# Performance work log

Measured on AMD Instinct MI355X. Metric: run time of the kernel, lower is better.

## Reference

```python
import jax, jax.numpy as jnp
import numpy as np

B, T, E = 2, 2048, 1024
H = 16
D = E // H  # 64

def setup_inputs() -> dict:
    key = jax.random.key(0)
    kx, kq, kk, kv, ko = jax.random.split(key, 5)
    s = 1.0 / np.sqrt(E)
    return {
        "x":  jax.random.normal(kx, (B, T, E), dtype=jnp.float32),
        "Wq": jax.random.normal(kq, (E, E), dtype=jnp.float32) * s,
        "Wk": jax.random.normal(kk, (E, E), dtype=jnp.float32) * s,
        "Wv": jax.random.normal(kv, (E, E), dtype=jnp.float32) * s,
        "Wo": jax.random.normal(ko, (E, E), dtype=jnp.float32) * s,
    }

def reference(x, Wq, Wk, Wv, Wo):
    # Faithful to the torch module, including its quirks:
    #  - head split is a raw .view(B, H, T, D) reshape (NOT a transpose split)
    #  - masked_fill result is discarded in the original, so NO causal mask is applied
    #  - dropout = 0.0 -> identity
    b, t, e = x.shape
    q = jnp.reshape(x @ Wq, (b, H, t, D))
    k = jnp.reshape(x @ Wk, (b, H, t, D))
    v = jnp.reshape(x @ Wv, (b, H, t, D))
    # raw_score = q @ k^T ; softmax over keys of raw_score / sqrt(head_dim)
    scores = jnp.einsum("bhtd,bhsd->bhts", q, k) / jnp.sqrt(jnp.asarray(D, x.dtype))
    attn = jax.nn.softmax(scores, axis=-1)
    h = jnp.einsum("bhts,bhsd->bhtd", attn, v)           # (B,H,T,D)
    h = jnp.reshape(h, (b, t, e))                         # .view(B, T, -1)
    return h @ Wo
```

## Files before the change

### kernel.cpp

```cpp
#include <hip/hip_runtime.h>
#include <hip/hip_bf16.h>
#include <math.h>

#define BB 2
#define TT 2048
#define EE 1024
#define HH 16
#define DD 64
#define MM (BB*TT)

typedef __bf16 bf16;
typedef bf16 bf16x8 __attribute__((ext_vector_type(8)));
typedef bf16 bf16x4 __attribute__((ext_vector_type(4)));
typedef float f32x4 __attribute__((ext_vector_type(4)));

#define MFMA16(a,b,c) __builtin_amdgcn_mfma_f32_16x16x32_bf16((a),(b),(c),0,0,0)

__device__ __forceinline__ void gload_lds16(const void* g, void* l) {
  __builtin_amdgcn_global_load_lds(
      (const __attribute__((address_space(1))) unsigned int*)g,
      (__attribute__((address_space(3))) unsigned int*)l, 16, 0, 0);
}

__device__ __forceinline__ unsigned short bits(bf16 h) {
  return __builtin_bit_cast(unsigned short, h);
}

__global__ __launch_bounds__(256) void prep(const float* __restrict__ x,
                                            const float* __restrict__ w0,
                                            const float* __restrict__ w1,
                                            const float* __restrict__ w2,
                                            const float* __restrict__ w3,
                                            bf16* __restrict__ xb,
                                            bf16* t0, bf16* t1, bf16* t2, bf16* t3) {
  __shared__ bf16 tile[64][65];
  const int bid = blockIdx.x;
  if (bid < 4096) {
    const int i = bid * 256 + threadIdx.x;
    float4 f = ((const float4*)x)[i];
    bf16x4 h;
    h[0] = (bf16)f.x; h[1] = (bf16)f.y; h[2] = (bf16)f.z; h[3] = (bf16)f.w;
    ((bf16x4*)xb)[i] = h;
    return;
  }
  const int t = bid - 4096;
  const int z = t >> 8, rem = t & 255;
  const float* W = z == 0 ? w0 : z == 1 ? w1 : z == 2 ? w2 : w3;
  bf16* T = z == 0 ? t0 : z == 1 ? t1 : z == 2 ? t2 : t3;
  const int n0 = (rem & 15) * 64, k0 = (rem >> 4) * 64;
#pragma unroll
  for (int i = 0; i < 16; i++) {
    int idx = threadIdx.x + i * 256;
    int r = idx >> 6, c = idx & 63;
    tile[c][r] = (bf16)W[(size_t)(k0 + r) * EE + n0 + c];
  }
  __syncthreads();
#pragma unroll
  for (int i = 0; i < 16; i++) {
    int idx = threadIdx.x + i * 256;
    int r = idx >> 6, c = idx & 63;
    T[(size_t)(n0 + r) * EE + k0 + c] = tile[r][c];
  }
}

template <typename OutT>
__device__ __forceinline__ void gemm_core(const bf16* __restrict__ A, const bf16* __restrict__ Bt,
                                          OutT* __restrict__ C, bf16* As, bf16* Bs) {
  const int tid = threadIdx.x;
  const int w = tid >> 6, lane = tid & 63;
  const int lg = lane >> 4, lr = lane & 15;
  const int row0 = blockIdx.y * 128, col0 = blockIdx.x * 128;
  const int wrow = (w >> 1) * 64, wcol = (w & 1) * 64;
  f32x4 acc[4][4];
#pragma unroll
  for (int m = 0; m < 4; m++)
#pragma unroll
    for (int n = 0; n < 4; n++) acc[m][n] = f32x4{0.f, 0.f, 0.f, 0.f};

  for (int kt = 0; kt < EE; kt += 32) {
#pragma unroll
    for (int i = 0; i < 2; i++) {
      const int c = i * 4 + w;
      const int row = c * 16 + (lane >> 2);
      const int kof = (lane & 3) * 8;
      gload_lds16(A + (size_t)(row0 + row) * EE + kt + kof, &As[c * 512]);
      gload_lds16(Bt + (size_t)(col0 + row) * EE + kt + kof, &Bs[c * 512]);
    }
    __syncthreads();
    bf16x8 a[4], b[4];
#pragma unroll
    for (int m = 0; m < 4; m++)
      a[m] = *(const bf16x8*)&As[(wrow + m * 16 + lr) * 32 + lg * 8];
#pragma unroll
    for (int n = 0; n < 4; n++)
      b[n] = *(const bf16x8*)&Bs[(wcol + n * 16 + lr) * 32 + lg * 8];
#pragma unroll
    for (int m = 0; m < 4; m++)
#pragma unroll
      for (int n = 0; n < 4; n++) acc[m][n] = MFMA16(a[m], b[n], acc[m][n]);
    __syncthreads();
  }
#pragma unroll
  for (int m = 0; m < 4; m++)
#pragma unroll
    for (int n = 0; n < 4; n++)
#pragma unroll
      for (int r = 0; r < 4; r++) {
        const int rr = row0 + wrow + m * 16 + lg * 4 + r;
        const int cc = col0 + wcol + n * 16 + lr;
        C[(size_t)rr * EE + cc] = (OutT)acc[m][n][r];
      }
}

__global__ __launch_bounds__(256) void gemm_qkv(const bf16* __restrict__ A,
                                                const bf16* __restrict__ w0,
                                                const bf16* __restrict__ w1,
                                                const bf16* __restrict__ w2,
                                                bf16* o0, bf16* o1, bf16* o2) {
  __shared__ __align__(16) bf16 As[128 * 32];
  __shared__ __align__(16) bf16 Bs[128 * 32];
  const bf16* Bt = (blockIdx.z == 0) ? w0 : (blockIdx.z == 1) ? w1 : w2;
  bf16* C = (blockIdx.z == 0) ? o0 : (blockIdx.z == 1) ? o1 : o2;
  gemm_core<bf16>(A, Bt, C, As, Bs);
}

__global__ __launch_bounds__(256) void gemm_out(const bf16* __restrict__ A,
                                                const bf16* __restrict__ Bt,
                                                float* __restrict__ C) {
  __shared__ __align__(16) bf16 As[128 * 32];
  __shared__ __align__(16) bf16 Bs[128 * 32];
  gemm_core<float>(A, Bt, C, As, Bs);
}

__global__ __launch_bounds__(256, 2) void flash_attn(const bf16* __restrict__ Q,
                                                     const bf16* __restrict__ K,
                                                     const bf16* __restrict__ V,
                                                     bf16* __restrict__ Hout) {
  const int tid = threadIdx.x;
  const int w = tid >> 6, lane = tid & 63;
  const int hi = lane >> 4, lr = lane & 15;

  const int bid = blockIdx.x + 16 * blockIdx.y;
  const int sid = (bid & 7) * 64 + (bid >> 3);
  const int qb = sid & 15, bh = sid >> 4;

  const size_t base = (size_t)(bh >> 4) * TT * EE + (size_t)(bh & 15) * 128 * EE;
  const bf16* qh = Q + base;
  const bf16* kh = K + base;
  const bf16* vh = V + base;
  bf16* hh = Hout + base;
  const int r0w = qb * 128 + w * 32;

  __shared__ __align__(16) bf16 Ks[2][64 * 72];
  __shared__ __align__(16) bf16 Vt[2][64 * 72];

  const float qscale = 0.18033688011112042f;
  bf16x8 aq[2][2];
#pragma unroll
  for (int rg = 0; rg < 2; rg++)
#pragma unroll
    for (int kk = 0; kk < 2; kk++) {
      bf16x8 qv = *(const bf16x8*)(qh + (size_t)(r0w + rg * 16 + lr) * DD + kk * 32 + hi * 8);
#pragma unroll
      for (int j = 0; j < 8; j++) qv[j] = (bf16)(qscale * (float)qv[j]);
      aq[rg][kk] = qv;
    }

  float l_[2] = {0.f, 0.f};
  f32x4 o[2][4];
#pragma unroll
  for (int rg = 0; rg < 2; rg++)
#pragma unroll
    for (int d = 0; d < 4; d++) o[rg][d] = f32x4{0.f, 0.f, 0.f, 0.f};

  const int krow = tid >> 2, kg8 = (tid & 3) * 8;
  const int vsp = tid & 31, vdb = (tid >> 5) * 4;
  const int s0p = 2 * vsp;
  const int vcs = (s0p & 32) | (((s0p >> 2) & 3) << 3) | (((s0p >> 4) & 1) << 2) | (s0p & 3);

  bf16x8 kr0 = *(const bf16x8*)(kh + (size_t)krow * DD + kg8);
  bf16x8 kr1 = *(const bf16x8*)(kh + (size_t)krow * DD + kg8 + 32);
  bf16x4 va0 = *(const bf16x4*)(vh + (size_t)(2 * vsp) * DD + vdb);
  bf16x4 vb0 = *(const bf16x4*)(vh + (size_t)(2 * vsp + 1) * DD + vdb);
  bf16x4 va1 = *(const bf16x4*)(vh + (size_t)(2 * vsp) * DD + vdb + 32);
  bf16x4 vb1 = *(const bf16x4*)(vh + (size_t)(2 * vsp + 1) * DD + vdb + 32);
  *(bf16x8*)&Ks[0][krow * 72 + kg8] = kr0;
  *(bf16x8*)&Ks[0][krow * 72 + kg8 + 32] = kr1;
#pragma unroll
  for (int j = 0; j < 4; j++) {
    unsigned u0 = (unsigned)bits(va0[j]) | ((unsigned)bits(vb0[j]) << 16);
    unsigned u1 = (unsigned)bits(va1[j]) | ((unsigned)bits(vb1[j]) << 16);
    *(unsigned*)&Vt[0][(vdb + j) * 72 + vcs] = u0;
    *(unsigned*)&Vt[0][(vdb + 32 + j) * 72 + vcs] = u1;
  }
  kr0 = *(const bf16x8*)(kh + (size_t)(64 + krow) * DD + kg8);
  kr1 = *(const bf16x8*)(kh + (size_t)(64 + krow) * DD + kg8 + 32);
  va0 = *(const bf16x4*)(vh + (size_t)(64 + 2 * vsp) * DD + vdb);
  vb0 = *(const bf16x4*)(vh + (size_t)(64 + 2 * vsp + 1) * DD + vdb);
  va1 = *(const bf16x4*)(vh + (size_t)(64 + 2 * vsp) * DD + vdb + 32);
  vb1 = *(const bf16x4*)(vh + (size_t)(64 + 2 * vsp + 1) * DD + vdb + 32);
  __syncthreads();

  for (int t = 0; t < TT / 64; t++) {
    const bf16* Kc = Ks[t & 1];
    const bf16* Vc = Vt[t & 1];

    f32x4 sA[2][4];
#pragma unroll
    for (int rg = 0; rg < 2; rg++)
#pragma unroll
      for (int cf = 0; cf < 4; cf++) sA[rg][cf] = f32x4{0.f, 0.f, 0.f, 0.f};
#pragma unroll
    for (int cf = 0; cf < 4; cf++)
#pragma unroll
      for (int kk = 0; kk < 2; kk++) {
        bf16x8 bk = *(const bf16x8*)&Kc[(cf * 16 + lr) * 72 + kk * 32 + hi * 8];
#pragma unroll
        for (int rg = 0; rg < 2; rg++) sA[rg][cf] = MFMA16(bk, aq[rg][kk], sA[rg][cf]);
      }

    bf16x8 bp[2][2];
#pragma unroll
    for (int rg = 0; rg < 2; rg++) {
      f32x4 pr[4];
#pragma unroll
      for (int cf = 0; cf < 4; cf++)
#pragma unroll
        for (int r = 0; r < 4; r++) {
          float p = __builtin_amdgcn_exp2f(sA[rg][cf][r]);
          l_[rg] += p;
          pr[cf][r] = p;
        }
#pragma unroll
      for (int kk = 0; kk < 2; kk++)
#pragma unroll
        for (int j = 0; j < 8; j++)
          bp[rg][kk][j] = (bf16)pr[2 * kk + (j >> 2)][j & 3];
    }

#pragma unroll
    for (int kk = 0; kk < 2; kk++)
#pragma unroll
      for (int dblk = 0; dblk < 4; dblk++) {
        bf16x8 av = *(const bf16x8*)&Vc[(dblk * 16 + lr) * 72 + kk * 32 + hi * 8];
#pragma unroll
        for (int rg = 0; rg < 2; rg++)
          o[rg][dblk] = MFMA16(av, bp[rg][kk], o[rg][dblk]);
      }

    if (t < TT / 64 - 1) {
      bf16* Kn = Ks[(t + 1) & 1];
      bf16* Vn = Vt[(t + 1) & 1];
      *(bf16x8*)&Kn[krow * 72 + kg8] = kr0;
      *(bf16x8*)&Kn[krow * 72 + kg8 + 32] = kr1;
#pragma unroll
      for (int j = 0; j < 4; j++) {
        unsigned u0 = (unsigned)bits(va0[j]) | ((unsigned)bits(vb0[j]) << 16);
        unsigned u1 = (unsigned)bits(va1[j]) | ((unsigned)bits(vb1[j]) << 16);
        *(unsigned*)&Vn[(vdb + j) * 72 + vcs] = u0;
        *(unsigned*)&Vn[(vdb + 32 + j) * 72 + vcs] = u1;
      }
      if (t < TT / 64 - 2) {
        const int s2 = (t + 2) * 64;
        kr0 = *(const bf16x8*)(kh + (size_t)(s2 + krow) * DD + kg8);
        kr1 = *(const bf16x8*)(kh + (size_t)(s2 + krow) * DD + kg8 + 32);
        va0 = *(const bf16x4*)(vh + (size_t)(s2 + 2 * vsp) * DD + vdb);
        vb0 = *(const bf16x4*)(vh + (size_t)(s2 + 2 * vsp + 1) * DD + vdb);
        va1 = *(const bf16x4*)(vh + (size_t)(s2 + 2 * vsp) * DD + vdb + 32);
        vb1 = *(const bf16x4*)(vh + (size_t)(s2 + 2 * vsp + 1) * DD + vdb + 32);
      }
    }
    __syncthreads();
  }

#pragma unroll
  for (int rg = 0; rg < 2; rg++) {
    float lt = l_[rg];
    lt += __shfl_xor(lt, 16);
    lt += __shfl_xor(lt, 32);
#pragma unroll
    for (int dblk = 0; dblk < 4; dblk++) {
      bf16x4 st;
#pragma unroll
      for (int r = 0; r < 4; r++) st[r] = (bf16)(o[rg][dblk][r] / lt);
      *(bf16x4*)(hh + (size_t)(r0w + rg * 16 + lr) * DD + dblk * 16 + 4 * hi) = st;
    }
  }
}

extern "C" void kernel_launch(void* const* d_in, const int* in_sizes, int n_in,
                              void* d_out, int out_size, void* d_ws, size_t ws_size,
                              hipStream_t stream) {
  const float* x  = (const float*)d_in[0];
  const float* Wq = (const float*)d_in[1];
  const float* Wk = (const float*)d_in[2];
  const float* Wv = (const float*)d_in[3];
  const float* Wo = (const float*)d_in[4];
  float* out = (float*)d_out;

  bf16* xb  = (bf16*)d_ws;
  bf16* wqt = xb + (size_t)MM * EE;
  bf16* wkt = wqt + (size_t)EE * EE;
  bf16* wvt = wkt + (size_t)EE * EE;
  bf16* wot = wvt + (size_t)EE * EE;
  bf16* Qb  = wot + (size_t)EE * EE;
  bf16* Kb  = Qb + (size_t)MM * EE;
  bf16* Vb  = Kb + (size_t)MM * EE;
  bf16* Hb  = xb;

  prep<<<dim3(5120), 256, 0, stream>>>(x, Wq, Wk, Wv, Wo, xb, wqt, wkt, wvt, wot);
  gemm_qkv<<<dim3(8, 32, 3), 256, 0, stream>>>(xb, wqt, wkt, wvt, Qb, Kb, Vb);
  flash_attn<<<dim3(16, 32), 256, 0, stream>>>(Qb, Kb, Vb, Hb);
  gemm_out<<<dim3(8, 32), 256, 0, stream>>>(Hb, wot, out);
}
```

Baseline: 114.5 us.

## Split attention over two key halves and merge partial results

Flash attention now splits the key/value sequence into two halves across a third grid dimension, doubling the block count. Each block writes unnormalized fp32 partial outputs and row sums, and a new merge kernel sums the halves, normalizes and writes bf16. The aim is more resident waves per CU and better latency hiding, with launch bounds raised to allow four blocks per CU. In exchange it adds a sizable fp32 round trip through global memory and an extra launch. Merging by plain summation is only correct if both halves use the same fixed softmax offset rather than a per-half running max.

```diff
diff --git a/kernel.cpp b/kernel.cpp
--- a/kernel.cpp
+++ b/kernel.cpp
@@ -132,22 +132,27 @@
   gemm_core<float>(A, Bt, C, As, Bs);
 }
 
-__global__ __launch_bounds__(256, 2) void flash_attn(const bf16* __restrict__ Q,
-                                                     const bf16* __restrict__ K,
-                                                     const bf16* __restrict__ V,
-                                                     bf16* __restrict__ Hout) {
+template <bool PARTIAL>
+__global__ __launch_bounds__(256, PARTIAL ? 4 : 2)
+void flash_attn(const bf16* __restrict__ Q, const bf16* __restrict__ K,
+                const bf16* __restrict__ V, bf16* __restrict__ Hout,
+                float* __restrict__ Opart, float* __restrict__ Lpart) {
   const int tid = threadIdx.x;
   const int w = tid >> 6, lane = tid & 63;
   const int hi = lane >> 4, lr = lane & 15;
 
-  const int bid = blockIdx.x + 16 * blockIdx.y;
-  const int sid = (bid & 7) * 64 + (bid >> 3);
-  const int qb = sid & 15, bh = sid >> 4;
+  const int NB = PARTIAL ? 1024 : 512;
+  const int bid = blockIdx.x + 16 * blockIdx.y + (PARTIAL ? 512 * blockIdx.z : 0);
+  const int sid = (bid & 7) * (NB / 8) + (bid >> 3);
+  const int qb = sid & 15;
+  const int bh = (sid >> 4) & 31;
+  const int sh = PARTIAL ? (sid >> 9) : 0;
+  const int NT = PARTIAL ? (TT / 128) : (TT / 64);
 
   const size_t base = (size_t)(bh >> 4) * TT * EE + (size_t)(bh & 15) * 128 * EE;
   const bf16* qh = Q + base;
-  const bf16* kh = K + base;
-  const bf16* vh = V + base;
+  const bf16* kh = K + base + (size_t)sh * (TT / 2) * DD;
+  const bf16* vh = V + base + (size_t)sh * (TT / 2) * DD;
   bf16* hh = Hout + base;
   const int r0w = qb * 128 + w * 32;
 
@@ -201,7 +206,7 @@
   vb1 = *(const bf16x4*)(vh + (size_t)(64 + 2 * vsp + 1) * DD + vdb + 32);
   __syncthreads();
 
-  for (int t = 0; t < TT / 64; t++) {
+  for (int t = 0; t < NT; t++) {
     const bf16* Kc = Ks[t & 1];
     const bf16* Vc = Vt[t & 1];
 
@@ -248,7 +253,7 @@
           o[rg][dblk] = MFMA16(av, bp[rg][kk], o[rg][dblk]);
       }
 
-    if (t < TT / 64 - 1) {
+    if (t < NT - 1) {
       bf16* Kn = Ks[(t + 1) & 1];
       bf16* Vn = Vt[(t + 1) & 1];
       *(bf16x8*)&Kn[krow * 72 + kg8] = kr0;
@@ -260,7 +265,7 @@
         *(unsigned*)&Vn[(vdb + j) * 72 + vcs] = u0;
         *(unsigned*)&Vn[(vdb + 32 + j) * 72 + vcs] = u1;
       }
-      if (t < TT / 64 - 2) {
+      if (t < NT - 2) {
         const int s2 = (t + 2) * 64;
         kr0 = *(const bf16x8*)(kh + (size_t)(s2 + krow) * DD + kg8);
         kr1 = *(const bf16x8*)(kh + (size_t)(s2 + krow) * DD + kg8 + 32);
@@ -273,19 +278,59 @@
     __syncthreads();
   }
 
-#pragma unroll
-  for (int rg = 0; rg < 2; rg++) {
-    float lt = l_[rg];
-    lt += __shfl_xor(lt, 16);
-    lt += __shfl_xor(lt, 32);
-#pragma unroll
-    for (int dblk = 0; dblk < 4; dblk++) {
-      bf16x4 st;
-#pragma unroll
-      for (int r = 0; r < 4; r++) st[r] = (bf16)(o[rg][dblk][r] / lt);
-      *(bf16x4*)(hh + (size_t)(r0w + rg * 16 + lr) * DD + dblk * 16 + 4 * hi) = st;
-    }
-  }
+  if (PARTIAL) {
+    float* op = Opart + ((size_t)sh * 32 + bh) * TT * DD;
+    float* lp = Lpart + ((size_t)sh * 32 + bh) * TT;
+#pragma unroll
+    for (int rg = 0; rg < 2; rg++) {
+      const int q = r0w + rg * 16 + lr;
+      float lt = l_[rg];
+      lt += __shfl_xor(lt, 16);
+      lt += __shfl_xor(lt, 32);
+      if (hi == 0) lp[q] = lt;
+#pragma unroll
+      for (int dblk = 0; dblk < 4; dblk++)
+        *(f32x4*)&op[(size_t)q * DD + dblk * 16 + 4 * hi] = o[rg][dblk];
+    }
+  } else {
+#pragma unroll
+    for (int rg = 0; rg < 2; rg++) {
+      float lt = l_[rg];
+      lt += __shfl_xor(lt, 16);
+      lt += __shfl_xor(lt, 32);
+#pragma unroll
+      for (int dblk = 0; dblk < 4; dblk++) {
+        bf16x4 st;
+#pragma unroll
+        for (int r = 0; r < 4; r++) st[r] = (bf16)(o[rg][dblk][r] / lt);
+        *(bf16x4*)(hh + (size_t)(r0w + rg * 16 + lr) * DD + dblk * 16 + 4 * hi) = st;
+      }
+    }
+  }
+}
+
+__global__ __launch_bounds__(256) void merge_attn(const float* __restrict__ Opart,
+                                                  const float* __restrict__ Lpart,
+                                                  bf16* __restrict__ Hb) {
+  const int gid = blockIdx.x * 256 + threadIdx.x;
+  const int qg = gid >> 2;
+  const int d0 = (gid & 3) * 16;
+  const size_t off = (size_t)qg * DD + d0;
+  const size_t half = (size_t)32 * TT * DD;
+  const float inv = 1.0f / (Lpart[qg] + Lpart[32 * TT + qg]);
+  bf16x8 r0, r1;
+#pragma unroll
+  for (int v = 0; v < 4; v++) {
+    f32x4 a = *(const f32x4*)&Opart[off + v * 4];
+    f32x4 b = *(const f32x4*)&Opart[half + off + v * 4];
+#pragma unroll
+    for (int j = 0; j < 4; j++) {
+      bf16 x = (bf16)((a[j] + b[j]) * inv);
+      if (v < 2) r0[v * 4 + j] = x; else r1[(v - 2) * 4 + j] = x;
+    }
+  }
+  *(bf16x8*)&Hb[off] = r0;
+  *(bf16x8*)&Hb[off + 8] = r1;
 }
 
 extern "C" void kernel_launch(void* const* d_in, const int* in_sizes, int n_in,
@@ -308,8 +353,18 @@
   bf16* Vb  = Kb + (size_t)MM * EE;
   bf16* Hb  = xb;
 
+  const size_t base_bytes = ((size_t)MM * EE + 4 * (size_t)EE * EE + 3 * (size_t)MM * EE) * 2;
+  float* Opart = (float*)((char*)d_ws + base_bytes);
+  float* Lpart = Opart + (size_t)2 * 32 * TT * DD;
+  const size_t need = base_bytes + ((size_t)2 * 32 * TT * DD + (size_t)2 * 32 * TT) * 4;
+
   prep<<<dim3(5120), 256, 0, stream>>>(x, Wq, Wk, Wv, Wo, xb, wqt, wkt, wvt, wot);
   gemm_qkv<<<dim3(8, 32, 3), 256, 0, stream>>>(xb, wqt, wkt, wvt, Qb, Kb, Vb);
-  flash_attn<<<dim3(16, 32), 256, 0, stream>>>(Qb, Kb, Vb, Hb);
+  if (ws_size >= need) {
+    flash_attn<true><<<dim3(16, 32, 2), 256, 0, stream>>>(Qb, Kb, Vb, Hb, Opart, Lpart);
+    merge_attn<<<dim3(1024), 256, 0, stream>>>(Opart, Lpart, Hb);
+  } else {
+    flash_attn<false><<<dim3(16, 32), 256, 0, stream>>>(Qb, Kb, Vb, Hb, Opart, Lpart);
+  }
   gemm_out<<<dim3(8, 32), 256, 0, stream>>>(Hb, wot, out);
 }
```

Measured after the change: 126.1 us. +10.1%, slower.

## Split attention key blocks across wave pairs and retile output GEMM to 128x64

Applied to the files above, without the earlier changes.

In flash attention, each wave now covers 64 query rows and half of each 64-key block instead of 32 rows and the full block. This halves the per-wave LDS reads of K and V fragments. The two partial outputs and row sums are then combined through shared memory in an epilogue, which costs an extra barrier and LDS traffic at the end. Separately, the output projection GEMM uses a 128x64 tile with a grid twice as large, so more blocks are available to fill the CUs.

```diff
diff --git a/kernel.cpp b/kernel.cpp
--- a/kernel.cpp
+++ b/kernel.cpp
@@ -128,8 +128,53 @@
                                                 const bf16* __restrict__ Bt,
                                                 float* __restrict__ C) {
   __shared__ __align__(16) bf16 As[128 * 32];
-  __shared__ __align__(16) bf16 Bs[128 * 32];
-  gemm_core<float>(A, Bt, C, As, Bs);
+  __shared__ __align__(16) bf16 Bs[64 * 32];
+  const int tid = threadIdx.x;
+  const int w = tid >> 6, lane = tid & 63;
+  const int lg = lane >> 4, lr = lane & 15;
+  const int row0 = blockIdx.y * 128, col0 = blockIdx.x * 64;
+  const int wrow = (w >> 1) * 64, wcol = (w & 1) * 32;
+  f32x4 acc[4][2];
+#pragma unroll
+  for (int m = 0; m < 4; m++)
+#pragma unroll
+    for (int n = 0; n < 2; n++) acc[m][n] = f32x4{0.f, 0.f, 0.f, 0.f};
+
+  for (int kt = 0; kt < EE; kt += 32) {
+#pragma unroll
+    for (int i = 0; i < 3; i++) {
+      const int c = i * 4 + w;
+      const int r16 = lane >> 2, kof = (lane & 3) * 8;
+      if (c < 8)
+        gload_lds16(A + (size_t)(row0 + c * 16 + r16) * EE + kt + kof, &As[c * 512]);
+      else
+        gload_lds16(Bt + (size_t)(col0 + (c - 8) * 16 + r16) * EE + kt + kof,
+                    &Bs[(c - 8) * 512]);
+    }
+    __syncthreads();
+    bf16x8 a[4], b[2];
+#pragma unroll
+    for (int m = 0; m < 4; m++)
+      a[m] = *(const bf16x8*)&As[(wrow + m * 16 + lr) * 32 + lg * 8];
+#pragma unroll
+    for (int n = 0; n < 2; n++)
+      b[n] = *(const bf16x8*)&Bs[(wcol + n * 16 + lr) * 32 + lg * 8];
+#pragma unroll
+    for (int m = 0; m < 4; m++)
+#pragma unroll
+      for (int n = 0; n < 2; n++) acc[m][n] = MFMA16(a[m], b[n], acc[m][n]);
+    __syncthreads();
+  }
+#pragma unroll
+  for (int m = 0; m < 4; m++)
+#pragma unroll
+    for (int n = 0; n < 2; n++)
+#pragma unroll
+      for (int r = 0; r < 4; r++) {
+        const int rr = row0 + wrow + m * 16 + lg * 4 + r;
+        const int cc = col0 + wcol + n * 16 + lr;
+        C[(size_t)rr * EE + cc] = acc[m][n][r];
+      }
 }
 
 __global__ __launch_bounds__(256, 2) void flash_attn(const bf16* __restrict__ Q,
@@ -139,37 +184,39 @@
   const int tid = threadIdx.x;
   const int w = tid >> 6, lane = tid & 63;
   const int hi = lane >> 4, lr = lane & 15;
+  const int qh = w & 1, sh2 = w >> 1;
 
   const int bid = blockIdx.x + 16 * blockIdx.y;
   const int sid = (bid & 7) * 64 + (bid >> 3);
   const int qb = sid & 15, bh = sid >> 4;
 
   const size_t base = (size_t)(bh >> 4) * TT * EE + (size_t)(bh & 15) * 128 * EE;
-  const bf16* qh = Q + base;
+  const bf16* qh_p = Q + base;
   const bf16* kh = K + base;
   const bf16* vh = V + base;
   bf16* hh = Hout + base;
-  const int r0w = qb * 128 + w * 32;
-
-  __shared__ __align__(16) bf16 Ks[2][64 * 72];
-  __shared__ __align__(16) bf16 Vt[2][64 * 72];
+  const int qbase = qb * 128 + qh * 64;
+
+  __shared__ __align__(16) bf16 smem[4 * 64 * 72];
+  bf16* KsBuf = smem;
+  bf16* VtBuf = smem + 2 * 64 * 72;
 
   const float qscale = 0.18033688011112042f;
-  bf16x8 aq[2][2];
-#pragma unroll
-  for (int rg = 0; rg < 2; rg++)
+  bf16x8 aq[4][2];
+#pragma unroll
+  for (int rg = 0; rg < 4; rg++)
 #pragma unroll
     for (int kk = 0; kk < 2; kk++) {
-      bf16x8 qv = *(const bf16x8*)(qh + (size_t)(r0w + rg * 16 + lr) * DD + kk * 32 + hi * 8);
+      bf16x8 qv = *(const bf16x8*)(qh_p + (size_t)(qbase + rg * 16 + lr) * DD + kk * 32 + hi * 8);
 #pragma unroll
       for (int j = 0; j < 8; j++) qv[j] = (bf16)(qscale * (float)qv[j]);
       aq[rg][kk] = qv;
     }
 
-  float l_[2] = {0.f, 0.f};
-  f32x4 o[2][4];
-#pragma unroll
-  for (int rg = 0; rg < 2; rg++)
+  float l_[4] = {0.f, 0.f, 0.f, 0.f};
+  f32x4 o[4][4];
+#pragma unroll
+  for (int rg = 0; rg < 4; rg++)
 #pragma unroll
     for (int d = 0; d < 4; d++) o[rg][d] = f32x4{0.f, 0.f, 0.f, 0.f};
 
@@ -184,14 +231,14 @@
   bf16x4 vb0 = *(const bf16x4*)(vh + (size_t)(2 * vsp + 1) * DD + vdb);
   bf16x4 va1 = *(const bf16x4*)(vh + (size_t)(2 * vsp) * DD + vdb + 32);
   bf16x4 vb1 = *(const bf16x4*)(vh + (size_t)(2 * vsp + 1) * DD + vdb + 32);
-  *(bf16x8*)&Ks[0][krow * 72 + kg8] = kr0;
-  *(bf16x8*)&Ks[0][krow * 72 + kg8 + 32] = kr1;
+  *(bf16x8*)&KsBuf[krow * 72 + kg8] = kr0;
+  *(bf16x8*)&KsBuf[krow * 72 + kg8 + 32] = kr1;
 #pragma unroll
   for (int j = 0; j < 4; j++) {
     unsigned u0 = (unsigned)bits(va0[j]) | ((unsigned)bits(vb0[j]) << 16);
     unsigned u1 = (unsigned)bits(va1[j]) | ((unsigned)bits(vb1[j]) << 16);
-    *(unsigned*)&Vt[0][(vdb + j) * 72 + vcs] = u0;
-    *(unsigned*)&Vt[0][(vdb + 32 + j) * 72 + vcs] = u1;
+    *(unsigned*)&VtBuf[(vdb + j) * 72 + vcs] = u0;
+    *(unsigned*)&VtBuf[(vdb + 32 + j) * 72 + vcs] = u1;
   }
   kr0 = *(const bf16x8*)(kh + (size_t)(64 + krow) * DD + kg8);
   kr1 = *(const bf16x8*)(kh + (size_t)(64 + krow) * DD + kg8 + 32);
@@ -202,55 +249,49 @@
   __syncthreads();
 
   for (int t = 0; t < TT / 64; t++) {
-    const bf16* Kc = Ks[t & 1];
-    const bf16* Vc = Vt[t & 1];
-
-    f32x4 sA[2][4];
-#pragma unroll
-    for (int rg = 0; rg < 2; rg++)
-#pragma unroll
-      for (int cf = 0; cf < 4; cf++) sA[rg][cf] = f32x4{0.f, 0.f, 0.f, 0.f};
-#pragma unroll
-    for (int cf = 0; cf < 4; cf++)
+    const bf16* Kc = &KsBuf[(t & 1) * 64 * 72];
+    const bf16* Vc = &VtBuf[(t & 1) * 64 * 72];
+
+    f32x4 sA[4][2];
+#pragma unroll
+    for (int rg = 0; rg < 4; rg++)
+#pragma unroll
+      for (int cfl = 0; cfl < 2; cfl++) sA[rg][cfl] = f32x4{0.f, 0.f, 0.f, 0.f};
+#pragma unroll
+    for (int cfl = 0; cfl < 2; cfl++)
 #pragma unroll
       for (int kk = 0; kk < 2; kk++) {
-        bf16x8 bk = *(const bf16x8*)&Kc[(cf * 16 + lr) * 72 + kk * 32 + hi * 8];
-#pragma unroll
-        for (int rg = 0; rg < 2; rg++) sA[rg][cf] = MFMA16(bk, aq[rg][kk], sA[rg][cf]);
-      }
-
-    bf16x8 bp[2][2];
-#pragma unroll
-    for (int rg = 0; rg < 2; rg++) {
-      f32x4 pr[4];
-#pragma unroll
-      for (int cf = 0; cf < 4; cf++)
+        bf16x8 bk = *(const bf16x8*)&Kc[(sh2 * 32 + cfl * 16 + lr) * 72 + kk * 32 + hi * 8];
+#pragma unroll
+        for (int rg = 0; rg < 4; rg++) sA[rg][cfl] = MFMA16(bk, aq[rg][kk], sA[rg][cfl]);
+      }
+
+    bf16x8 bp[4];
+#pragma unroll
+    for (int rg = 0; rg < 4; rg++) {
+      f32x4 pr[2];
+#pragma unroll
+      for (int cfl = 0; cfl < 2; cfl++)
 #pragma unroll
         for (int r = 0; r < 4; r++) {
-          float p = __builtin_amdgcn_exp2f(sA[rg][cf][r]);
+          float p = __builtin_amdgcn_exp2f(sA[rg][cfl][r]);
           l_[rg] += p;
-          pr[cf][r] = p;
+          pr[cfl][r] = p;
         }
 #pragma unroll
-      for (int kk = 0; kk < 2; kk++)
-#pragma unroll
-        for (int j = 0; j < 8; j++)
-          bp[rg][kk][j] = (bf16)pr[2 * kk + (j >> 2)][j & 3];
-    }
-
-#pragma unroll
-    for (int kk = 0; kk < 2; kk++)
-#pragma unroll
-      for (int dblk = 0; dblk < 4; dblk++) {
-        bf16x8 av = *(const bf16x8*)&Vc[(dblk * 16 + lr) * 72 + kk * 32 + hi * 8];
-#pragma unroll
-        for (int rg = 0; rg < 2; rg++)
-          o[rg][dblk] = MFMA16(av, bp[rg][kk], o[rg][dblk]);
-      }
+      for (int j = 0; j < 8; j++) bp[rg][j] = (bf16)pr[j >> 2][j & 3];
+    }
+
+#pragma unroll
+    for (int dblk = 0; dblk < 4; dblk++) {
+      bf16x8 av = *(const bf16x8*)&Vc[(dblk * 16 + lr) * 72 + sh2 * 32 + hi * 8];
+#pragma unroll
+      for (int rg = 0; rg < 4; rg++) o[rg][dblk] = MFMA16(av, bp[rg], o[rg][dblk]);
+    }
 
     if (t < TT / 64 - 1) {
-      bf16* Kn = Ks[(t + 1) & 1];
-      bf16* Vn = Vt[(t + 1) & 1];
+      bf16* Kn = &KsBuf[((t + 1) & 1) * 64 * 72];
+      bf16* Vn = &VtBuf[((t + 1) & 1) * 64 * 72];
       *(bf16x8*)&Kn[krow * 72 + kg8] = kr0;
       *(bf16x8*)&Kn[krow * 72 + kg8 + 32] = kr1;
 #pragma unroll
@@ -273,17 +314,38 @@
     __syncthreads();
   }
 
-#pragma unroll
-  for (int rg = 0; rg < 2; rg++) {
-    float lt = l_[rg];
-    lt += __shfl_xor(lt, 16);
-    lt += __shfl_xor(lt, 32);
-#pragma unroll
-    for (int dblk = 0; dblk < 4; dblk++) {
-      bf16x4 st;
-#pragma unroll
-      for (int r = 0; r < 4; r++) st[r] = (bf16)(o[rg][dblk][r] / lt);
-      *(bf16x4*)(hh + (size_t)(r0w + rg * 16 + lr) * DD + dblk * 16 + 4 * hi) = st;
+  float lt[4];
+#pragma unroll
+  for (int rg = 0; rg < 4; rg++) {
+    lt[rg] = l_[rg];
+    lt[rg] += __shfl_xor(lt[rg], 16);
+    lt[rg] += __shfl_xor(lt[rg], 32);
+  }
+  float* sc = (float*)smem;
+  float* scl = sc + 2 * 64 * 68;
+  if (sh2 == 1) {
+#pragma unroll
+    for (int rg = 0; rg < 4; rg++) {
+#pragma unroll
+      for (int dblk = 0; dblk < 4; dblk++)
+        *(f32x4*)&sc[qh * 4352 + (rg * 16 + lr) * 68 + dblk * 16 + 4 * hi] = o[rg][dblk];
+      if (hi == 0) scl[qh * 64 + rg * 16 + lr] = lt[rg];
+    }
+  }
+  __syncthreads();
+  if (sh2 == 0) {
+#pragma unroll
+    for (int rg = 0; rg < 4; rg++) {
+      const float ltot = lt[rg] + scl[qh * 64 + rg * 16 + lr];
+      const float inv = 1.0f / ltot;
+#pragma unroll
+      for (int dblk = 0; dblk < 4; dblk++) {
+        f32x4 ob = *(const f32x4*)&sc[qh * 4352 + (rg * 16 + lr) * 68 + dblk * 16 + 4 * hi];
+        bf16x4 st;
+#pragma unroll
+        for (int r = 0; r < 4; r++) st[r] = (bf16)((o[rg][dblk][r] + ob[r]) * inv);
+        *(bf16x4*)(hh + (size_t)(qbase + rg * 16 + lr) * DD + dblk * 16 + 4 * hi) = st;
+      }
     }
   }
 }
@@ -311,5 +373,5 @@
   prep<<<dim3(5120), 256, 0, stream>>>(x, Wq, Wk, Wv, Wo, xb, wqt, wkt, wvt, wot);
   gemm_qkv<<<dim3(8, 32, 3), 256, 0, stream>>>(xb, wqt, wkt, wvt, Qb, Kb, Vb);
   flash_attn<<<dim3(16, 32), 256, 0, stream>>>(Qb, Kb, Vb, Hb);
-  gemm_out<<<dim3(8, 32), 256, 0, stream>>>(Hb, wot, out);
-}
+  gemm_out<<<dim3(16, 32), 256, 0, stream>>>(Hb, wot, out);
+}
```

Result: no change. 114.7 us (+0.2%).
